# Kernel optimization log

Measured on AMD Instinct MI355X. Metric: run time of the kernel, lower is better.

Reference implementation:

```python
import jax, jax.numpy as jnp
import numpy as np

MEL = 80  # seq2seq_dim


def gru_step(x, h, Wg, bg, Wc, bc):
    """TF GRUCell: gates=[r,u], new_h = u*h + (1-u)*c."""
    gates = jax.nn.sigmoid(jnp.concatenate([x, h], axis=-1) @ Wg + bg)
    r, u = jnp.split(gates, 2, axis=-1)
    c = jnp.tanh(jnp.concatenate([x, r * h], axis=-1) @ Wc + bc)
    return u * h + (1.0 - u) * c


def setup_inputs() -> dict:
    key = jax.random.key(0)
    B, T_enc, D_enc = 128, 1024, 256
    n_styles, style_dim = 10, 256
    reduc, T_dec = 5, 250
    ks = jax.random.split(key, 20)
    rn = lambda k, shape, s=0.05: jax.random.normal(k, shape, jnp.float32) * s
    return {
        "encoder_output": rn(ks[0], (B, T_enc, D_enc), 1.0),
        "inp_mask": jax.random.randint(ks[1], (B,), 1, T_enc + 1, dtype=jnp.int32),
        "inp_att": jax.nn.softmax(rn(ks[2], (B, n_styles), 1.0), axis=-1),
        "style_token": rn(ks[3], (n_styles, style_dim)),
        # decoder prenet 80->256->128
        "pre_W1": rn(ks[4], (MEL, 256)), "pre_b1": jnp.zeros((256,), jnp.float32),
        "pre_W2": rn(ks[5], (256, 128)), "pre_b2": jnp.zeros((128,), jnp.float32),
        # attention GRU cell: input = [context(256), prenet(128)] = 384, hidden 256
        "att_Wg": rn(ks[6], (384 + 256, 512)), "att_bg": jnp.ones((512,), jnp.float32),
        "att_Wc": rn(ks[7], (384 + 256, 256)), "att_bc": jnp.zeros((256,), jnp.float32),
        # Bahdanau attention (depth 256)
        "attn_Wk": rn(ks[8], (256, 256)), "attn_bk": jnp.zeros((256,), jnp.float32),
        "attn_Wq": rn(ks[9], (256, 256)), "attn_bq": jnp.zeros((256,), jnp.float32),
        "attn_v": rn(ks[10], (256,)),
        # dec_input dense: [att_out(256), weighting_context(256)] -> 256
        "deci_W": rn(ks[11], (512, 256)), "deci_b": jnp.zeros((256,), jnp.float32),
        # two residual GRU decoder layers (hidden 256)
        "dec1_Wg": rn(ks[12], (512, 512)), "dec1_bg": jnp.ones((512,), jnp.float32),
        "dec1_Wc": rn(ks[13], (512, 256)), "dec1_bc": jnp.zeros((256,), jnp.float32),
        "dec2_Wg": rn(ks[14], (512, 512)), "dec2_bg": jnp.ones((512,), jnp.float32),
        "dec2_Wc": rn(ks[15], (512, 256)), "dec2_bc": jnp.zeros((256,), jnp.float32),
        # output projection 256 -> mel*reduc
        "out_W": rn(ks[16], (256, MEL * reduc)), "out_b": jnp.zeros((MEL * reduc,), jnp.float32),
        "decode_time_steps": T_dec,
    }


def reference(encoder_output, inp_mask, inp_att, style_token,
              pre_W1, pre_b1, pre_W2, pre_b2,
              att_Wg, att_bg, att_Wc, att_bc,
              attn_Wk, attn_bk, attn_Wq, attn_bq, attn_v,
              deci_W, deci_b,
              dec1_Wg, dec1_bg, dec1_Wc, dec1_bc,
              dec2_Wg, dec2_bg, dec2_Wc, dec2_bc,
              out_W, out_b, decode_time_steps):
    B, T_enc, D = encoder_output.shape
    reduc = out_W.shape[1] // MEL
    # precompute attention keys and mask (done once in TF AttentionModule)
    keys = encoder_output @ attn_Wk + attn_bk                       # [B, T_enc, 256]
    mask = jnp.arange(T_enc)[None, :] < inp_mask[:, None]           # [B, T_enc]
    sentence_style = inp_att @ style_token                          # [B, 256]
    abs_style = jnp.abs(sentence_style)

    carry0 = (
        jnp.zeros((B, 256), jnp.float32),   # att GRU state
        jnp.zeros((B, 256), jnp.float32),   # dec GRU layer 1 state
        jnp.zeros((B, 256), jnp.float32),   # dec GRU layer 2 state
        jnp.zeros((B, 256), jnp.float32),   # last context
        jnp.zeros((B, MEL), jnp.float32),   # go frame / last output
    )

    def step(carry, _):
        h_att, h1, h2, ctx, last_out = carry
        # decoder prenet (dropout inactive, training=False)
        p = jax.nn.relu(last_out @ pre_W1 + pre_b1)
        p = jax.nn.relu(p @ pre_W2 + pre_b2)
        # attention RNN
        h_att = gru_step(jnp.concatenate([ctx, p], axis=-1), h_att,
                         att_Wg, att_bg, att_Wc, att_bc)
        # Bahdanau attention with query = attention cell state
        q = h_att @ attn_Wq + attn_bq                               # [B, 256]
        e = jnp.einsum('btd,d->bt', jnp.tanh(keys + q[:, None, :]), attn_v)
        e = jnp.where(mask, e, -1e9)
        alpha = jax.nn.softmax(e, axis=-1)                          # [B, T_enc]
        context = jnp.einsum('bt,btd->bd', alpha, encoder_output)   # [B, 256]
        # style-weighted context
        wctx = context + sentence_style
        weight_per = jnp.mean(abs_style / (jnp.abs(context) + abs_style))
        # decoder RNN: dense then 2 residual GRU layers
        dec_in = jnp.concatenate([h_att, wctx], axis=-1) @ deci_W + deci_b
        h1 = gru_step(dec_in, h1, dec1_Wg, dec1_bg, dec1_Wc, dec1_bc)
        o1 = h1 + dec_in
        h2 = gru_step(o1, h2, dec2_Wg, dec2_bg, dec2_Wc, dec2_bc)
        o2 = h2 + o1
        dense_out = o2 @ out_W + out_b                              # [B, mel*reduc]
        new_out = dense_out[:, -MEL:]
        return (h_att, h1, h2, context, new_out), (dense_out, alpha, weight_per)

    _, (dense_outs, alphas, weight_pers) = jax.lax.scan(
        step, carry0, None, length=decode_time_steps)
    # [T_dec, B, mel*reduc] -> [B, T_dec*reduc, mel]
    seq2seq_output = jnp.transpose(dense_outs, (1, 0, 2)).reshape(
        B, decode_time_steps * reduc, MEL)
    return seq2seq_output, alphas, weight_pers
```

## Files before the change

kernel.cpp:

```cpp
#include <hip/hip_runtime.h>
#include <cstdint>
#include <cstddef>


#define TDEC   250
#define BATCH  128

#define ALPHA_OFF  ((size_t)12800000)
#define WP_OFF     ((size_t)45568000)

#define WS_WACC_B   ((size_t)0)
#define WS_WGT_B    ((size_t)4096)
#define WGT_ELEMS   1658880
#define WS_KEYS_B   (WS_WGT_B + (size_t)WGT_ELEMS * 2)
#define WS_ENC_B    (WS_KEYS_B + (size_t)33554432 * 2)

#define OFF_PRE_W1   0
#define OFF_PRE_W2   20480
#define OFF_ATT_WG   53248
#define OFF_ATT_WC   380928
#define OFF_ATT_WCH  479232
#define OFF_ATTN_WQ  544768
#define OFF_DECI_W   610304
#define OFF_DEC1_WG  741376
#define OFF_DEC1_WC  1003520
#define OFF_DEC1_WCH 1069056
#define OFF_DEC2_WG  1134592
#define OFF_DEC2_WC  1396736
#define OFF_DEC2_WCH 1462272
#define OFF_OUT_WP   1527808

__device__ inline float bf2f(unsigned short u){
    return __uint_as_float(((unsigned int)u) << 16);
}
__device__ inline unsigned short f2bf(float f){
    unsigned int u = __float_as_uint(f);
    u = (u + 0x7fffu + ((u >> 16) & 1u)) >> 16;
    return (unsigned short)u;
}
__device__ inline float ftanh(float x){
    float e = __expf(2.f * x);
    return 1.f - 2.f * __builtin_amdgcn_rcpf(e + 1.f);
}
__device__ inline float fsig(float x){
    return __builtin_amdgcn_rcpf(1.f + __expf(-x));
}

template<int K, int N, int PARTS>
__device__ inline void gemv_part(const unsigned short* __restrict__ W,
                                 const float* __restrict__ x,
                                 float* __restrict__ scratch, int tid)
{
    constexpr int CH   = N / 8;
    constexpr int LG   = (CH == 16) ? 4 : (CH == 32) ? 5 : 6;
    constexpr int KCNT = K / PARTS;
    static_assert(KCNT * PARTS == K, "K must divide");
    static_assert(CH * PARTS <= 1024, "too many threads");
    const int chunk = tid & (CH - 1);
    const int part  = tid >> LG;
    if (PARTS == (1024 >> LG) || part < PARTS){
        const uint4* Wp = (const uint4*)W + (size_t)(part * KCNT) * (N / 8) + chunk;
        const float* xp = x + part * KCNT;
        float a0=0.f,a1=0.f,a2=0.f,a3=0.f,a4=0.f,a5=0.f,a6=0.f,a7=0.f;
        #pragma unroll 8
        for (int k = 0; k < KCNT; k++){
            uint4 w = Wp[(size_t)k * (N / 8)];
            float xv = xp[k];
            a0 = fmaf(__uint_as_float(w.x << 16),         xv, a0);
            a1 = fmaf(__uint_as_float(w.x & 0xffff0000u), xv, a1);
            a2 = fmaf(__uint_as_float(w.y << 16),         xv, a2);
            a3 = fmaf(__uint_as_float(w.y & 0xffff0000u), xv, a3);
            a4 = fmaf(__uint_as_float(w.z << 16),         xv, a4);
            a5 = fmaf(__uint_as_float(w.z & 0xffff0000u), xv, a5);
            a6 = fmaf(__uint_as_float(w.w << 16),         xv, a6);
            a7 = fmaf(__uint_as_float(w.w & 0xffff0000u), xv, a7);
        }
        float4* s4 = (float4*)(scratch + part * N + chunk * 8);
        s4[0] = float4{a0, a1, a2, a3};
        s4[1] = float4{a4, a5, a6, a7};
    }
}

template<int N, int PARTS>
__device__ inline float red_parts(const float* __restrict__ scratch, int n){
    float s = 0.f;
    #pragma unroll
    for (int p = 0; p < PARTS; p++) s += scratch[p * N + n];
    return s;
}

__global__ void k_cvt_flat(const float* __restrict__ src, unsigned short* __restrict__ dst, int n){
    int i = blockIdx.x * 256 + threadIdx.x;
    if (i < n) dst[i] = f2bf(src[i]);
}
__global__ void k_cvt_pad(const float* __restrict__ src, unsigned short* __restrict__ dst){
    int i = blockIdx.x * 256 + threadIdx.x;
    int k = i >> 9, n = i & 511;
    dst[i] = (n < 400) ? f2bf(src[k * 400 + n]) : (unsigned short)0;
}

__global__ __launch_bounds__(256) void k_keys(const float* __restrict__ enc,
                                              const float* __restrict__ Wk,
                                              const float* __restrict__ bk,
                                              unsigned short* __restrict__ keysT)
{
    __shared__ __align__(16) float Wt[64 * 256];
    __shared__ float At[64 * 64];
    __shared__ unsigned short tileT[256 * 68];
    const int tid = threadIdx.x;
    const size_t row0 = (size_t)blockIdx.x * 64;
    const int dq = tid & 63;
    const int rg = tid >> 6;

    float4 acc[16];
    #pragma unroll
    for (int i = 0; i < 16; i++) acc[i] = float4{0.f, 0.f, 0.f, 0.f};

    for (int k0 = 0; k0 < 256; k0 += 64){
        __syncthreads();
        #pragma unroll
        for (int i = 0; i < 64; i++)
            Wt[i * 256 + tid] = Wk[(size_t)(k0 + i) * 256 + tid];
        #pragma unroll
        for (int i = 0; i < 16; i++){
            int idx = tid + i * 256;
            int r = idx >> 6, kk = idx & 63;
            At[idx] = enc[(row0 + r) * 256 + k0 + kk];
        }
        __syncthreads();
        for (int kk = 0; kk < 64; kk++){
            float4 w = ((const float4*)Wt)[kk * 64 + dq];
            #pragma unroll
            for (int rr = 0; rr < 16; rr++){
                float a = At[(rg * 16 + rr) * 64 + kk];
                acc[rr].x += a * w.x; acc[rr].y += a * w.y;
                acc[rr].z += a * w.z; acc[rr].w += a * w.w;
            }
        }
    }
    float4 bb = ((const float4*)bk)[dq];
    __syncthreads();
    #pragma unroll
    for (int rr = 0; rr < 16; rr++){
        int t_loc = rg * 16 + rr;
        #pragma unroll
        for (int c = 0; c < 4; c++){
            float val = (&acc[rr].x)[c] + (&bb.x)[c];
            int d = dq * 4 + c;
            tileT[d * 68 + t_loc] = f2bf(val);
        }
    }
    __syncthreads();
    const int b_ = (int)(row0 >> 10);
    const int t0 = (int)(row0 & 1023);
    #pragma unroll
    for (int i = 0; i < 16; i++){
        int flat = tid + i * 256;
        int d = flat >> 4, tq = flat & 15;
        ushort4 v = *(const ushort4*)&tileT[d * 68 + tq * 4];
        *(ushort4*)&keysT[(((size_t)(b_ * 256 + d)) << 10) + t0 + tq * 4] = v;
    }
}

struct KParams {
    const int *imask; const float *inp_att; const float *style_tok;
    const float *pre_b1, *pre_b2, *att_bg, *att_bc, *attn_bq, *attn_v;
    const float *deci_b, *dec1_bg, *dec1_bc, *dec2_bg, *dec2_bc, *out_b;
    const unsigned short *wgt;
    const unsigned short *keysT;
    const unsigned short *encb;
    float *wacc; float *out;
};

__global__ __launch_bounds__(1024, 1) void k_main(KParams p)
{
    __shared__ __align__(16) float scr [8192];
    __shared__ __align__(16) float scr2[8192];
    __shared__ float xa[640];
    __shared__ float xg[512];
    __shared__ float xr[256];
    __shared__ float xd[512];
    __shared__ float g_l[512], cx_l[256];
    __shared__ float h_att[256], h1[256], h2[256];
    __shared__ float p1_l[256], dci[256], o1_l[256], o2_l[256];
    __shared__ float stylel[256], astylel[256], v_l[256], q_l[256];
    __shared__ float e_l[1024];
    __shared__ float last_o[80];
    __shared__ float red[16];

    const int tid = threadIdx.x;
    const int b   = blockIdx.x;
    const int mlen = p.imask[b];
    const unsigned short* W = p.wgt;

    if (tid < 256){
        h_att[tid] = 0.f; h1[tid] = 0.f; h2[tid] = 0.f;
        float s = 0.f;
        #pragma unroll
        for (int k = 0; k < 10; k++) s += p.inp_att[b * 10 + k] * p.style_tok[k * 256 + tid];
        stylel[tid] = s; astylel[tid] = fabsf(s);
        v_l[tid] = p.attn_v[tid];
        xa[tid] = 0.f;
        xa[384 + tid] = 0.f;
    }
    if (tid < 80) last_o[tid] = 0.f;
    __syncthreads();

    for (int s = 0; s < TDEC; s++){
        gemv_part<80, 256, 16>(W + OFF_PRE_W1, last_o, scr, tid);
        __syncthreads();
        if (tid < 256)
            p1_l[tid] = fmaxf(p.pre_b1[tid] + red_parts<256,16>(scr, tid), 0.f);
        __syncthreads();

        gemv_part<256, 128, 64>(W + OFF_PRE_W2, p1_l, scr, tid);
        __syncthreads();
        if (tid < 128)
            xa[256 + tid] = fmaxf(p.pre_b2[tid] + red_parts<128,64>(scr, tid), 0.f);
        __syncthreads();

        gemv_part<640, 512, 16>(W + OFF_ATT_WG, xa, scr,  tid);
        gemv_part<384, 256, 32>(W + OFF_ATT_WC, xa, scr2, tid);
        __syncthreads();
        if (tid < 512){
            float g = fsig(p.att_bg[tid] + red_parts<512,16>(scr, tid));
            g_l[tid] = g;
            if (tid < 256) xr[tid] = g * h_att[tid];
        } else if (tid < 768){
            int n = tid - 512;
            cx_l[n] = p.att_bc[n] + red_parts<256,32>(scr2, n);
        }
        __syncthreads();

        gemv_part<256, 256, 32>(W + OFF_ATT_WCH, xr, scr, tid);
        __syncthreads();
        if (tid < 256){
            float c = ftanh(cx_l[tid] + red_parts<256,32>(scr, tid));
            float u = g_l[256 + tid];
            float h = u * h_att[tid] + (1.f - u) * c;
            h_att[tid] = h;
            xa[384 + tid] = h;
            xd[tid] = h;
        }
        __syncthreads();

        gemv_part<256, 256, 32>(W + OFF_ATTN_WQ, h_att, scr, tid);
        __syncthreads();
        if (tid < 256) q_l[tid] = p.attn_bq[tid] + red_parts<256,32>(scr, tid);
        __syncthreads();

        {
            const int tc   = tid & 127;
            const int part = tid >> 7;
            float acc0=0.f,acc1=0.f,acc2=0.f,acc3=0.f,acc4=0.f,acc5=0.f,acc6=0.f,acc7=0.f;
            if (tc * 8 < mlen){
                const unsigned short* kp = p.keysT + (((size_t)b) << 18)
                                         + ((size_t)(part * 32) << 10) + tc * 8;
                #pragma unroll 16
                for (int dd = 0; dd < 32; dd++){
                    uint4 kv = *(const uint4*)(kp + ((size_t)dd << 10));
                    int d = part * 32 + dd;
                    float qd = q_l[d], vd = v_l[d];
                    acc0 = fmaf(ftanh(__uint_as_float(kv.x << 16)         + qd), vd, acc0);
                    acc1 = fmaf(ftanh(__uint_as_float(kv.x & 0xffff0000u) + qd), vd, acc1);
                    acc2 = fmaf(ftanh(__uint_as_float(kv.y << 16)         + qd), vd, acc2);
                    acc3 = fmaf(ftanh(__uint_as_float(kv.y & 0xffff0000u) + qd), vd, acc3);
                    acc4 = fmaf(ftanh(__uint_as_float(kv.z << 16)         + qd), vd, acc4);
                    acc5 = fmaf(ftanh(__uint_as_float(kv.z & 0xffff0000u) + qd), vd, acc5);
                    acc6 = fmaf(ftanh(__uint_as_float(kv.w << 16)         + qd), vd, acc6);
                    acc7 = fmaf(ftanh(__uint_as_float(kv.w & 0xffff0000u) + qd), vd, acc7);
                }
            }
            float4* s4 = (float4*)(scr + part * 1024 + tc * 8);
            s4[0] = float4{acc0, acc1, acc2, acc3};
            s4[1] = float4{acc4, acc5, acc6, acc7};
        }
        __syncthreads();
        float av = 0.f;
        if (tid < mlen){
            float s8 = 0.f;
            #pragma unroll
            for (int pp = 0; pp < 8; pp++) s8 += scr[pp * 1024 + tid];
            av = __expf(s8);
        }
        {
            float ws = av;
            #pragma unroll
            for (int off = 32; off; off >>= 1) ws += __shfl_xor(ws, off, 64);
            if ((tid & 63) == 0) red[tid >> 6] = ws;
        }
        __syncthreads();
        {
            float tot = 0.f;
            #pragma unroll
            for (int i = 0; i < 16; i++) tot += red[i];
            float alpha = av * __builtin_amdgcn_rcpf(tot);
            e_l[tid] = alpha;
            __builtin_nontemporal_store(alpha,
                &p.out[ALPHA_OFF + (size_t)s * 131072 + ((size_t)b << 10) + tid]);
        }
        __syncthreads();

        {
            const int dc = tid & 31;
            const int tp = tid >> 5;
            float acc0=0.f,acc1=0.f,acc2=0.f,acc3=0.f,acc4=0.f,acc5=0.f,acc6=0.f,acc7=0.f;
            const unsigned short* er = p.encb + (((size_t)b) << 18) + dc * 8;
            #pragma unroll 8
            for (int t = tp; t < mlen; t += 32){
                uint4 ev4 = *(const uint4*)(er + ((size_t)t << 8));
                float al = e_l[t];
                acc0 = fmaf(al, __uint_as_float(ev4.x << 16),         acc0);
                acc1 = fmaf(al, __uint_as_float(ev4.x & 0xffff0000u), acc1);
                acc2 = fmaf(al, __uint_as_float(ev4.y << 16),         acc2);
                acc3 = fmaf(al, __uint_as_float(ev4.y & 0xffff0000u), acc3);
                acc4 = fmaf(al, __uint_as_float(ev4.z << 16),         acc4);
                acc5 = fmaf(al, __uint_as_float(ev4.z & 0xffff0000u), acc5);
                acc6 = fmaf(al, __uint_as_float(ev4.w << 16),         acc6);
                acc7 = fmaf(al, __uint_as_float(ev4.w & 0xffff0000u), acc7);
            }
            float4* s4 = (float4*)(scr + tp * 256 + dc * 8);
            s4[0] = float4{acc0, acc1, acc2, acc3};
            s4[1] = float4{acc4, acc5, acc6, acc7};
        }
        __syncthreads();
        if (tid < 256){
            float cs = red_parts<256,32>(scr, tid);
            xa[tid] = cs;
            xd[256 + tid] = cs + stylel[tid];
            float wpv = astylel[tid] * __builtin_amdgcn_rcpf(fabsf(cs) + astylel[tid]);
            #pragma unroll
            for (int off = 32; off; off >>= 1) wpv += __shfl_xor(wpv, off, 64);
            if ((tid & 63) == 0) atomicAdd(&p.wacc[s], wpv);
        }
        __syncthreads();

        gemv_part<512, 256, 32>(W + OFF_DECI_W, xd, scr, tid);
        __syncthreads();
        if (tid < 256){
            float d = p.deci_b[tid] + red_parts<256,32>(scr, tid);
            dci[tid] = d;
            xg[tid] = d; xg[256 + tid] = h1[tid];
        }
        __syncthreads();

        gemv_part<512, 512, 16>(W + OFF_DEC1_WG, xg, scr,  tid);
        gemv_part<256, 256, 32>(W + OFF_DEC1_WC, xg, scr2, tid);
        __syncthreads();
        if (tid < 512){
            float g = fsig(p.dec1_bg[tid] + red_parts<512,16>(scr, tid));
            g_l[tid] = g;
            if (tid < 256) xr[tid] = g * h1[tid];
        } else if (tid < 768){
            int n = tid - 512;
            cx_l[n] = p.dec1_bc[n] + red_parts<256,32>(scr2, n);
        }
        __syncthreads();

        gemv_part<256, 256, 32>(W + OFF_DEC1_WCH, xr, scr, tid);
        __syncthreads();
        if (tid < 256){
            float c = ftanh(cx_l[tid] + red_parts<256,32>(scr, tid));
            float u = g_l[256 + tid];
            float hn = u * h1[tid] + (1.f - u) * c;
            h1[tid] = hn;
            float o1 = hn + dci[tid];
            o1_l[tid] = o1;
            xg[tid] = o1; xg[256 + tid] = h2[tid];
        }
        __syncthreads();

        gemv_part<512, 512, 16>(W + OFF_DEC2_WG, xg, scr,  tid);
        gemv_part<256, 256, 32>(W + OFF_DEC2_WC, xg, scr2, tid);
        __syncthreads();
        if (tid < 512){
            float g = fsig(p.dec2_bg[tid] + red_parts<512,16>(scr, tid));
            g_l[tid] = g;
            if (tid < 256) xr[tid] = g * h2[tid];
        } else if (tid < 768){
            int n = tid - 512;
            cx_l[n] = p.dec2_bc[n] + red_parts<256,32>(scr2, n);
        }
        __syncthreads();

        gemv_part<256, 256, 32>(W + OFF_DEC2_WCH, xr, scr, tid);
        __syncthreads();
        if (tid < 256){
            float c = ftanh(cx_l[tid] + red_parts<256,32>(scr, tid));
            float u = g_l[256 + tid];
            float hn = u * h2[tid] + (1.f - u) * c;
            h2[tid] = hn;
            o2_l[tid] = hn + o1_l[tid];
        }
        __syncthreads();

        gemv_part<256, 512, 16>(W + OFF_OUT_WP, o2_l, scr, tid);
        __syncthreads();
        if (tid < 400){
            float val = p.out_b[tid] + red_parts<512,16>(scr, tid);
            __builtin_nontemporal_store(val,
                &p.out[(size_t)b * 100000 + (size_t)s * 400 + tid]);
            if (tid >= 320) last_o[tid - 320] = val;
        }
        __syncthreads();
    }
}

__global__ void k_final(const float* __restrict__ wacc, float* __restrict__ out)
{
    int i = threadIdx.x;
    if (i < TDEC) out[WP_OFF + i] = wacc[i] * (1.0f / 32768.0f);
}

extern "C" void kernel_launch(void* const* d_in, const int* in_sizes, int n_in,
                              void* d_out, int out_size, void* d_ws, size_t ws_size,
                              hipStream_t stream)
{
    const float* enc        = (const float*)d_in[0];
    const int*   imask      = (const int*)  d_in[1];
    const float* inp_att    = (const float*)d_in[2];
    const float* style_tok  = (const float*)d_in[3];
    const float* pre_W1     = (const float*)d_in[4];
    const float* pre_b1     = (const float*)d_in[5];
    const float* pre_W2     = (const float*)d_in[6];
    const float* pre_b2     = (const float*)d_in[7];
    const float* att_Wg     = (const float*)d_in[8];
    const float* att_bg     = (const float*)d_in[9];
    const float* att_Wc     = (const float*)d_in[10];
    const float* att_bc     = (const float*)d_in[11];
    const float* attn_Wk    = (const float*)d_in[12];
    const float* attn_bk    = (const float*)d_in[13];
    const float* attn_Wq    = (const float*)d_in[14];
    const float* attn_bq    = (const float*)d_in[15];
    const float* attn_v     = (const float*)d_in[16];
    const float* deci_W     = (const float*)d_in[17];
    const float* deci_b     = (const float*)d_in[18];
    const float* dec1_Wg    = (const float*)d_in[19];
    const float* dec1_bg    = (const float*)d_in[20];
    const float* dec1_Wc    = (const float*)d_in[21];
    const float* dec1_bc    = (const float*)d_in[22];
    const float* dec2_Wg    = (const float*)d_in[23];
    const float* dec2_bg    = (const float*)d_in[24];
    const float* dec2_Wc    = (const float*)d_in[25];
    const float* dec2_bc    = (const float*)d_in[26];
    const float* out_W      = (const float*)d_in[27];
    const float* out_b      = (const float*)d_in[28];

    float*          wacc  = (float*)((char*)d_ws + WS_WACC_B);
    unsigned short* wgt   = (unsigned short*)((char*)d_ws + WS_WGT_B);
    unsigned short* keysT = (unsigned short*)((char*)d_ws + WS_KEYS_B);
    unsigned short* encb  = (unsigned short*)((char*)d_ws + WS_ENC_B);
    float* out = (float*)d_out;

    hipMemsetAsync(d_ws, 0, 1024, stream);

    auto cvt = [&](const float* src, size_t off, int n){
        k_cvt_flat<<<(n + 255) / 256, 256, 0, stream>>>(src, wgt + off, n);
    };
    cvt(pre_W1,  OFF_PRE_W1,   80 * 256);
    cvt(pre_W2,  OFF_PRE_W2,  256 * 128);
    cvt(att_Wg,  OFF_ATT_WG,  640 * 512);
    cvt(att_Wc,  OFF_ATT_WC,  640 * 256);
    cvt(attn_Wq, OFF_ATTN_WQ, 256 * 256);
    cvt(deci_W,  OFF_DECI_W,  512 * 256);
    cvt(dec1_Wg, OFF_DEC1_WG, 512 * 512);
    cvt(dec1_Wc, OFF_DEC1_WC, 512 * 256);
    cvt(dec2_Wg, OFF_DEC2_WG, 512 * 512);
    cvt(dec2_Wc, OFF_DEC2_WC, 512 * 256);
    k_cvt_pad<<<(256 * 512) / 256, 256, 0, stream>>>(out_W, wgt + OFF_OUT_WP);

    k_cvt_flat<<<(33554432 + 255) / 256, 256, 0, stream>>>(enc, encb, 33554432);

    k_keys<<<2048, 256, 0, stream>>>(enc, attn_Wk, attn_bk, keysT);

    KParams kp{imask, inp_att, style_tok,
               pre_b1, pre_b2, att_bg, att_bc, attn_bq, attn_v,
               deci_b, dec1_bg, dec1_bc, dec2_bg, dec2_bc, out_b,
               wgt, keysT, encb, wacc, out};
    k_main<<<BATCH, 1024, 0, stream>>>(kp);

    k_final<<<1, 256, 0, stream>>>(wacc, out);
}
```

Measured before the change: 23.70 ms.

## Split each batch row across two workgroups with global-memory pair handshakes

The persistent decoder kernel now runs two 512-thread workgroups per batch element instead of one 1024-thread workgroup. Each half computes its share of the GEMV output columns (or K-rows, for the dec2 and output layers) and its half of the attention time range. The halves exchange partial results through a global comm buffer and spin on per-pair flags. The dec2 gate weights are row-permuted so the K-split fits the concatenated input. This spreads the sequential recurrence over twice as many CUs to cut per-step latency, but adds about nine cross-workgroup syncs per step through L2, and it relies on both halves being co-resident so the spin-wait cannot deadlock.

```diff
diff --git a/kernel.cpp b/kernel.cpp
--- a/kernel.cpp
+++ b/kernel.cpp
@@ -10,10 +10,24 @@
 #define WP_OFF     ((size_t)45568000)
 
 #define WS_WACC_B   ((size_t)0)
-#define WS_WGT_B    ((size_t)4096)
+#define WS_FLAG_B   ((size_t)1024)
+#define WS_COMM_B   ((size_t)4096)
+#define COMM_STRIDE 4096
+#define WS_WGT_B    (WS_COMM_B + (size_t)256 * COMM_STRIDE * 4)
 #define WGT_ELEMS   1658880
 #define WS_KEYS_B   (WS_WGT_B + (size_t)WGT_ELEMS * 2)
 #define WS_ENC_B    (WS_KEYS_B + (size_t)33554432 * 2)
+
+#define CO_E0 0
+#define CO_E1 128
+#define CO_E2 192
+#define CO_E3 576
+#define CO_E4 960
+#define CO_E5 1024
+#define CO_E6 1280
+#define CO_E7 1408
+#define CO_E8 1792
+#define CO_E9 2688
 
 #define OFF_PRE_W1   0
 #define OFF_PRE_W2   20480
@@ -30,9 +44,6 @@
 #define OFF_DEC2_WCH 1462272
 #define OFF_OUT_WP   1527808
 
-__device__ inline float bf2f(unsigned short u){
-    return __uint_as_float(((unsigned int)u) << 16);
-}
 __device__ inline unsigned short f2bf(float f){
     unsigned int u = __float_as_uint(f);
     u = (u + 0x7fffu + ((u >> 16) & 1u)) >> 16;
@@ -46,25 +57,42 @@
     return __builtin_amdgcn_rcpf(1.f + __expf(-x));
 }
 
-template<int K, int N, int PARTS>
-__device__ inline void gemv_part(const unsigned short* __restrict__ W,
-                                 const float* __restrict__ x,
-                                 float* __restrict__ scratch, int tid)
+__device__ inline void cput(float* cm, int i, float v){
+    __hip_atomic_store(cm + i, v, __ATOMIC_RELAXED, __HIP_MEMORY_SCOPE_AGENT);
+}
+__device__ inline float cget(const float* cm, int i){
+    return __hip_atomic_load(cm + i, __ATOMIC_RELAXED, __HIP_MEMORY_SCOPE_AGENT);
+}
+__device__ inline void pair_wait(int* flags, int fm, int fo, int T, int tid){
+    __syncthreads();
+    if (tid == 0){
+        __hip_atomic_store(&flags[fm], T, __ATOMIC_RELAXED, __HIP_MEMORY_SCOPE_AGENT);
+        asm volatile("" ::: "memory");
+        while (__hip_atomic_load(&flags[fo], __ATOMIC_RELAXED, __HIP_MEMORY_SCOPE_AGENT) < T)
+            __builtin_amdgcn_s_sleep(1);
+    }
+    __syncthreads();
+}
+
+template<int K, int NFULL, int NW, int PARTS>
+__device__ inline void gemv_h(const unsigned short* __restrict__ W,
+                              const float* __restrict__ x,
+                              float* __restrict__ scratch, int tid)
 {
-    constexpr int CH   = N / 8;
-    constexpr int LG   = (CH == 16) ? 4 : (CH == 32) ? 5 : 6;
+    constexpr int CH = NW / 8;
+    constexpr int LG = (CH == 8) ? 3 : (CH == 16) ? 4 : (CH == 32) ? 5 : 6;
     constexpr int KCNT = K / PARTS;
     static_assert(KCNT * PARTS == K, "K must divide");
-    static_assert(CH * PARTS <= 1024, "too many threads");
+    static_assert(CH * PARTS <= 512, "too many threads");
     const int chunk = tid & (CH - 1);
     const int part  = tid >> LG;
-    if (PARTS == (1024 >> LG) || part < PARTS){
-        const uint4* Wp = (const uint4*)W + (size_t)(part * KCNT) * (N / 8) + chunk;
+    if (PARTS == (512 >> LG) || part < PARTS){
+        const uint4* Wp = (const uint4*)W + (size_t)(part * KCNT) * (NFULL / 8) + chunk;
         const float* xp = x + part * KCNT;
         float a0=0.f,a1=0.f,a2=0.f,a3=0.f,a4=0.f,a5=0.f,a6=0.f,a7=0.f;
         #pragma unroll 8
         for (int k = 0; k < KCNT; k++){
-            uint4 w = Wp[(size_t)k * (N / 8)];
+            uint4 w = Wp[(size_t)k * (NFULL / 8)];
             float xv = xp[k];
             a0 = fmaf(__uint_as_float(w.x << 16),         xv, a0);
             a1 = fmaf(__uint_as_float(w.x & 0xffff0000u), xv, a1);
@@ -75,17 +103,17 @@
             a6 = fmaf(__uint_as_float(w.w << 16),         xv, a6);
             a7 = fmaf(__uint_as_float(w.w & 0xffff0000u), xv, a7);
         }
-        float4* s4 = (float4*)(scratch + part * N + chunk * 8);
+        float4* s4 = (float4*)(scratch + part * NW + chunk * 8);
         s4[0] = float4{a0, a1, a2, a3};
         s4[1] = float4{a4, a5, a6, a7};
     }
 }
 
-template<int N, int PARTS>
+template<int NW, int PARTS>
 __device__ inline float red_parts(const float* __restrict__ scratch, int n){
     float s = 0.f;
     #pragma unroll
-    for (int p = 0; p < PARTS; p++) s += scratch[p * N + n];
+    for (int p = 0; p < PARTS; p++) s += scratch[p * NW + n];
     return s;
 }
 
@@ -97,6 +125,14 @@
     int i = blockIdx.x * 256 + threadIdx.x;
     int k = i >> 9, n = i & 511;
     dst[i] = (n < 400) ? f2bf(src[k * 400 + n]) : (unsigned short)0;
+}
+__global__ void k_cvt_wg2(const float* __restrict__ src, unsigned short* __restrict__ dst){
+    int i = blockIdx.x * 256 + threadIdx.x;
+    int r = i >> 9, n = i & 511;
+    int c = r >> 7;
+    int nc = (c == 1) ? 2 : (c == 2) ? 1 : c;
+    int nr = nc * 128 + (r & 127);
+    dst[nr * 512 + n] = f2bf(src[i]);
 }
 
 __global__ __launch_bounds__(256) void k_keys(const float* __restrict__ enc,
@@ -169,239 +205,299 @@
     const unsigned short *wgt;
     const unsigned short *keysT;
     const unsigned short *encb;
-    float *wacc; float *out;
+    float *wacc; float *comm; int *flags; float *out;
 };
 
-__global__ __launch_bounds__(1024, 1) void k_main(KParams p)
+__global__ __launch_bounds__(512, 4) void k_main(KParams p)
 {
-    __shared__ __align__(16) float scr [8192];
-    __shared__ __align__(16) float scr2[8192];
+    __shared__ __align__(16) float scr [4096];
+    __shared__ __align__(16) float scr2[4096];
     __shared__ float xa[640];
-    __shared__ float xg[512];
-    __shared__ float xr[256];
-    __shared__ float xd[512];
+    __shared__ float xbuf[512];
     __shared__ float g_l[512], cx_l[256];
-    __shared__ float h_att[256], h1[256], h2[256];
-    __shared__ float p1_l[256], dci[256], o1_l[256], o2_l[256];
+    __shared__ float h1[256], h2[256], dci[256], o1_l[256], o2loc[128];
+    __shared__ float p1_l[256];
     __shared__ float stylel[256], astylel[256], v_l[256], q_l[256];
-    __shared__ float e_l[1024];
+    __shared__ float e_l[512];
     __shared__ float last_o[80];
     __shared__ float red[16];
 
     const int tid = threadIdx.x;
-    const int b   = blockIdx.x;
+    const int b   = blockIdx.x >> 1;
+    const int h   = blockIdx.x & 1;
     const int mlen = p.imask[b];
     const unsigned short* W = p.wgt;
 
+    float* cm = p.comm + (size_t)(2 * b + h) * COMM_STRIDE;
+    const float* co = p.comm + (size_t)(2 * b + (1 - h)) * COMM_STRIDE;
+    const int fm = 2 * b + h, fo = 2 * b + (1 - h);
+    int seq = 0;
+
     if (tid < 256){
-        h_att[tid] = 0.f; h1[tid] = 0.f; h2[tid] = 0.f;
+        xa[384 + tid] = 0.f;
+        xa[tid] = 0.f;
+        h1[tid] = 0.f; h2[tid] = 0.f;
         float s = 0.f;
         #pragma unroll
         for (int k = 0; k < 10; k++) s += p.inp_att[b * 10 + k] * p.style_tok[k * 256 + tid];
         stylel[tid] = s; astylel[tid] = fabsf(s);
         v_l[tid] = p.attn_v[tid];
-        xa[tid] = 0.f;
-        xa[384 + tid] = 0.f;
     }
     if (tid < 80) last_o[tid] = 0.f;
     __syncthreads();
 
     for (int s = 0; s < TDEC; s++){
-        gemv_part<80, 256, 16>(W + OFF_PRE_W1, last_o, scr, tid);
-        __syncthreads();
+        gemv_h<80, 256, 128, 16>(W + OFF_PRE_W1 + h * 128, last_o, scr, tid);
+        __syncthreads();
+        if (tid < 128){
+            float v = fmaxf(p.pre_b1[h * 128 + tid] + red_parts<128,16>(scr, tid), 0.f);
+            p1_l[h * 128 + tid] = v;
+            cput(cm, CO_E0 + tid, v);
+        }
+        pair_wait(p.flags, fm, fo, ++seq, tid);
+        if (tid < 128) p1_l[(1 - h) * 128 + tid] = cget(co, CO_E0 + tid);
+        __syncthreads();
+
+        gemv_h<256, 128, 64, 64>(W + OFF_PRE_W2 + h * 64, p1_l, scr, tid);
+        __syncthreads();
+        if (tid < 64){
+            float v = fmaxf(p.pre_b2[h * 64 + tid] + red_parts<64,64>(scr, tid), 0.f);
+            xa[256 + h * 64 + tid] = v;
+            cput(cm, CO_E1 + tid, v);
+        }
+        pair_wait(p.flags, fm, fo, ++seq, tid);
+        if (tid < 64) xa[256 + (1 - h) * 64 + tid] = cget(co, CO_E1 + tid);
+        __syncthreads();
+
+        gemv_h<640, 512, 256, 16>(W + OFF_ATT_WG + h * 256, xa, scr,  tid);
+        gemv_h<384, 256, 128, 32>(W + OFF_ATT_WC + h * 128, xa, scr2, tid);
+        __syncthreads();
+        if (tid < 256){
+            float g = fsig(p.att_bg[h * 256 + tid] + red_parts<256,16>(scr, tid));
+            g_l[h * 256 + tid] = g;
+            cput(cm, CO_E2 + tid, g);
+        }
+        if (tid < 128){
+            float cx = p.att_bc[h * 128 + tid] + red_parts<128,32>(scr2, tid);
+            cx_l[h * 128 + tid] = cx;
+            cput(cm, CO_E2 + 256 + tid, cx);
+        }
+        pair_wait(p.flags, fm, fo, ++seq, tid);
+        if (tid < 256) g_l[(1 - h) * 256 + tid] = cget(co, CO_E2 + tid);
+        if (tid < 128) cx_l[(1 - h) * 128 + tid] = cget(co, CO_E2 + 256 + tid);
+        __syncthreads();
+
+        if (tid < 256) xbuf[tid] = g_l[tid] * xa[384 + tid];
+        __syncthreads();
+        gemv_h<256, 256, 128, 32>(W + OFF_ATT_WCH + h * 128, xbuf, scr, tid);
+        __syncthreads();
+        if (tid < 128){
+            int n = h * 128 + tid;
+            float c = ftanh(cx_l[n] + red_parts<128,32>(scr, tid));
+            float u = g_l[256 + n];
+            xa[384 + n] = u * xa[384 + n] + (1.f - u) * c;
+        }
+        __syncthreads();
+
+        gemv_h<128, 256, 256, 16>(W + OFF_ATTN_WQ + (size_t)(h * 128) * 256,
+                                  &xa[384 + h * 128], scr2, tid);
+        __syncthreads();
+        if (tid < 128) cput(cm, CO_E3 + tid, xa[384 + h * 128 + tid]);
+        if (tid < 256) cput(cm, CO_E3 + 128 + tid, red_parts<256,16>(scr2, tid));
+        pair_wait(p.flags, fm, fo, ++seq, tid);
+        if (tid < 128) xa[384 + (1 - h) * 128 + tid] = cget(co, CO_E3 + tid);
         if (tid < 256)
-            p1_l[tid] = fmaxf(p.pre_b1[tid] + red_parts<256,16>(scr, tid), 0.f);
-        __syncthreads();
-
-        gemv_part<256, 128, 64>(W + OFF_PRE_W2, p1_l, scr, tid);
-        __syncthreads();
-        if (tid < 128)
-            xa[256 + tid] = fmaxf(p.pre_b2[tid] + red_parts<128,64>(scr, tid), 0.f);
-        __syncthreads();
-
-        gemv_part<640, 512, 16>(W + OFF_ATT_WG, xa, scr,  tid);
-        gemv_part<384, 256, 32>(W + OFF_ATT_WC, xa, scr2, tid);
-        __syncthreads();
-        if (tid < 512){
-            float g = fsig(p.att_bg[tid] + red_parts<512,16>(scr, tid));
-            g_l[tid] = g;
-            if (tid < 256) xr[tid] = g * h_att[tid];
-        } else if (tid < 768){
-            int n = tid - 512;
-            cx_l[n] = p.att_bc[n] + red_parts<256,32>(scr2, n);
-        }
-        __syncthreads();
-
-        gemv_part<256, 256, 32>(W + OFF_ATT_WCH, xr, scr, tid);
-        __syncthreads();
-        if (tid < 256){
-            float c = ftanh(cx_l[tid] + red_parts<256,32>(scr, tid));
-            float u = g_l[256 + tid];
-            float h = u * h_att[tid] + (1.f - u) * c;
-            h_att[tid] = h;
-            xa[384 + tid] = h;
-            xd[tid] = h;
-        }
-        __syncthreads();
-
-        gemv_part<256, 256, 32>(W + OFF_ATTN_WQ, h_att, scr, tid);
-        __syncthreads();
-        if (tid < 256) q_l[tid] = p.attn_bq[tid] + red_parts<256,32>(scr, tid);
+            q_l[tid] = p.attn_bq[tid] + red_parts<256,16>(scr2, tid) + cget(co, CO_E3 + 128 + tid);
         __syncthreads();
 
         {
-            const int tc   = tid & 127;
-            const int part = tid >> 7;
-            float acc0=0.f,acc1=0.f,acc2=0.f,acc3=0.f,acc4=0.f,acc5=0.f,acc6=0.f,acc7=0.f;
-            if (tc * 8 < mlen){
+            const int tc   = tid & 63;
+            const int part = tid >> 6;
+            float a0=0.f,a1=0.f,a2=0.f,a3=0.f,a4=0.f,a5=0.f,a6=0.f,a7=0.f;
+            if (h * 512 + tc * 8 < mlen){
                 const unsigned short* kp = p.keysT + (((size_t)b) << 18)
-                                         + ((size_t)(part * 32) << 10) + tc * 8;
+                                         + ((size_t)(part * 32) << 10) + h * 512 + tc * 8;
                 #pragma unroll 16
                 for (int dd = 0; dd < 32; dd++){
                     uint4 kv = *(const uint4*)(kp + ((size_t)dd << 10));
                     int d = part * 32 + dd;
                     float qd = q_l[d], vd = v_l[d];
-                    acc0 = fmaf(ftanh(__uint_as_float(kv.x << 16)         + qd), vd, acc0);
-                    acc1 = fmaf(ftanh(__uint_as_float(kv.x & 0xffff0000u) + qd), vd, acc1);
-                    acc2 = fmaf(ftanh(__uint_as_float(kv.y << 16)         + qd), vd, acc2);
-                    acc3 = fmaf(ftanh(__uint_as_float(kv.y & 0xffff0000u) + qd), vd, acc3);
-                    acc4 = fmaf(ftanh(__uint_as_float(kv.z << 16)         + qd), vd, acc4);
-                    acc5 = fmaf(ftanh(__uint_as_float(kv.z & 0xffff0000u) + qd), vd, acc5);
-                    acc6 = fmaf(ftanh(__uint_as_float(kv.w << 16)         + qd), vd, acc6);
-                    acc7 = fmaf(ftanh(__uint_as_float(kv.w & 0xffff0000u) + qd), vd, acc7);
+                    a0 = fmaf(ftanh(__uint_as_float(kv.x << 16)         + qd), vd, a0);
+                    a1 = fmaf(ftanh(__uint_as_float(kv.x & 0xffff0000u) + qd), vd, a1);
+                    a2 = fmaf(ftanh(__uint_as_float(kv.y << 16)         + qd), vd, a2);
+                    a3 = fmaf(ftanh(__uint_as_float(kv.y & 0xffff0000u) + qd), vd, a3);
+                    a4 = fmaf(ftanh(__uint_as_float(kv.z << 16)         + qd), vd, a4);
+                    a5 = fmaf(ftanh(__uint_as_float(kv.z & 0xffff0000u) + qd), vd, a5);
+                    a6 = fmaf(ftanh(__uint_as_float(kv.w << 16)         + qd), vd, a6);
+                    a7 = fmaf(ftanh(__uint_as_float(kv.w & 0xffff0000u) + qd), vd, a7);
                 }
             }
-            float4* s4 = (float4*)(scr + part * 1024 + tc * 8);
-            s4[0] = float4{acc0, acc1, acc2, acc3};
-            s4[1] = float4{acc4, acc5, acc6, acc7};
-        }
-        __syncthreads();
-        float av = 0.f;
-        if (tid < mlen){
-            float s8 = 0.f;
+            float4* s4 = (float4*)(scr + part * 512 + tc * 8);
+            s4[0] = float4{a0, a1, a2, a3};
+            s4[1] = float4{a4, a5, a6, a7};
+        }
+        __syncthreads();
+        float av;
+        {
+            float e = 0.f;
             #pragma unroll
-            for (int pp = 0; pp < 8; pp++) s8 += scr[pp * 1024 + tid];
-            av = __expf(s8);
-        }
-        {
+            for (int pp = 0; pp < 8; pp++) e += scr[pp * 512 + tid];
+            av = (h * 512 + tid < mlen) ? __expf(e) : 0.f;
             float ws = av;
             #pragma unroll
             for (int off = 32; off; off >>= 1) ws += __shfl_xor(ws, off, 64);
             if ((tid & 63) == 0) red[tid >> 6] = ws;
         }
         __syncthreads();
+        if (tid == 0){
+            float dl = 0.f;
+            #pragma unroll
+            for (int i = 0; i < 8; i++) dl += red[i];
+            red[8] = dl;
+            cput(cm, CO_E4, dl);
+        }
+        pair_wait(p.flags, fm, fo, ++seq, tid);
         {
-            float tot = 0.f;
-            #pragma unroll
-            for (int i = 0; i < 16; i++) tot += red[i];
-            float alpha = av * __builtin_amdgcn_rcpf(tot);
+            float total = red[8] + cget(co, CO_E4);
+            float alpha = av * __builtin_amdgcn_rcpf(total);
             e_l[tid] = alpha;
             __builtin_nontemporal_store(alpha,
-                &p.out[ALPHA_OFF + (size_t)s * 131072 + ((size_t)b << 10) + tid]);
+                &p.out[ALPHA_OFF + (size_t)s * 131072 + ((size_t)b << 10) + h * 512 + tid]);
         }
         __syncthreads();
 
         {
             const int dc = tid & 31;
             const int tp = tid >> 5;
-            float acc0=0.f,acc1=0.f,acc2=0.f,acc3=0.f,acc4=0.f,acc5=0.f,acc6=0.f,acc7=0.f;
-            const unsigned short* er = p.encb + (((size_t)b) << 18) + dc * 8;
+            float a0=0.f,a1=0.f,a2=0.f,a3=0.f,a4=0.f,a5=0.f,a6=0.f,a7=0.f;
+            int mloc = mlen - h * 512;
+            if (mloc > 512) mloc = 512;
+            const unsigned short* er = p.encb + (((size_t)b) << 18)
+                                     + ((size_t)(h * 512) << 8) + dc * 8;
             #pragma unroll 8
-            for (int t = tp; t < mlen; t += 32){
+            for (int t = tp; t < mloc; t += 16){
                 uint4 ev4 = *(const uint4*)(er + ((size_t)t << 8));
                 float al = e_l[t];
-                acc0 = fmaf(al, __uint_as_float(ev4.x << 16),         acc0);
-                acc1 = fmaf(al, __uint_as_float(ev4.x & 0xffff0000u), acc1);
-                acc2 = fmaf(al, __uint_as_float(ev4.y << 16),         acc2);
-                acc3 = fmaf(al, __uint_as_float(ev4.y & 0xffff0000u), acc3);
-                acc4 = fmaf(al, __uint_as_float(ev4.z << 16),         acc4);
-                acc5 = fmaf(al, __uint_as_float(ev4.z & 0xffff0000u), acc5);
-                acc6 = fmaf(al, __uint_as_float(ev4.w << 16),         acc6);
-                acc7 = fmaf(al, __uint_as_float(ev4.w & 0xffff0000u), acc7);
+                a0 = fmaf(al, __uint_as_float(ev4.x << 16),         a0);
+                a1 = fmaf(al, __uint_as_float(ev4.x & 0xffff0000u), a1);
+                a2 = fmaf(al, __uint_as_float(ev4.y << 16),         a2);
+                a3 = fmaf(al, __uint_as_float(ev4.y & 0xffff0000u), a3);
+                a4 = fmaf(al, __uint_as_float(ev4.z << 16),         a4);
+                a5 = fmaf(al, __uint_as_float(ev4.z & 0xffff0000u), a5);
+                a6 = fmaf(al, __uint_as_float(ev4.w << 16),         a6);
+                a7 = fmaf(al, __uint_as_float(ev4.w & 0xffff0000u), a7);
             }
             float4* s4 = (float4*)(scr + tp * 256 + dc * 8);
-            s4[0] = float4{acc0, acc1, acc2, acc3};
-            s4[1] = float4{acc4, acc5, acc6, acc7};
-        }
-        __syncthreads();
+            s4[0] = float4{a0, a1, a2, a3};
+            s4[1] = float4{a4, a5, a6, a7};
+        }
+        __syncthreads();
+        if (tid < 256) cput(cm, CO_E5 + tid, red_parts<256,16>(scr, tid));
+        pair_wait(p.flags, fm, fo, ++seq, tid);
         if (tid < 256){
-            float cs = red_parts<256,32>(scr, tid);
+            float cs = red_parts<256,16>(scr, tid) + cget(co, CO_E5 + tid);
             xa[tid] = cs;
-            xd[256 + tid] = cs + stylel[tid];
-            float wpv = astylel[tid] * __builtin_amdgcn_rcpf(fabsf(cs) + astylel[tid]);
-            #pragma unroll
-            for (int off = 32; off; off >>= 1) wpv += __shfl_xor(wpv, off, 64);
-            if ((tid & 63) == 0) atomicAdd(&p.wacc[s], wpv);
-        }
-        __syncthreads();
-
-        gemv_part<512, 256, 32>(W + OFF_DECI_W, xd, scr, tid);
+            if (h == 0){
+                float wpv = astylel[tid] * __builtin_amdgcn_rcpf(fabsf(cs) + astylel[tid]);
+                #pragma unroll
+                for (int off = 32; off; off >>= 1) wpv += __shfl_xor(wpv, off, 64);
+                if ((tid & 63) == 0) atomicAdd(&p.wacc[s], wpv);
+            }
+        }
+        __syncthreads();
+
+        xbuf[tid] = (tid < 256) ? xa[384 + tid] : xa[tid - 256] + stylel[tid - 256];
+        __syncthreads();
+        gemv_h<512, 256, 128, 32>(W + OFF_DECI_W + h * 128, xbuf, scr, tid);
+        __syncthreads();
+        if (tid < 128){
+            float d = p.deci_b[h * 128 + tid] + red_parts<128,32>(scr, tid);
+            dci[h * 128 + tid] = d;
+            cput(cm, CO_E6 + tid, d);
+        }
+        pair_wait(p.flags, fm, fo, ++seq, tid);
+        if (tid < 128) dci[(1 - h) * 128 + tid] = cget(co, CO_E6 + tid);
+        __syncthreads();
+
+        xbuf[tid] = (tid < 256) ? dci[tid] : h1[tid - 256];
+        __syncthreads();
+        gemv_h<512, 512, 256, 16>(W + OFF_DEC1_WG + h * 256, xbuf, scr,  tid);
+        gemv_h<256, 256, 128, 32>(W + OFF_DEC1_WC + h * 128, xbuf, scr2, tid);
         __syncthreads();
         if (tid < 256){
-            float d = p.deci_b[tid] + red_parts<256,32>(scr, tid);
-            dci[tid] = d;
-            xg[tid] = d; xg[256 + tid] = h1[tid];
-        }
-        __syncthreads();
-
-        gemv_part<512, 512, 16>(W + OFF_DEC1_WG, xg, scr,  tid);
-        gemv_part<256, 256, 32>(W + OFF_DEC1_WC, xg, scr2, tid);
-        __syncthreads();
-        if (tid < 512){
-            float g = fsig(p.dec1_bg[tid] + red_parts<512,16>(scr, tid));
-            g_l[tid] = g;
-            if (tid < 256) xr[tid] = g * h1[tid];
-        } else if (tid < 768){
-            int n = tid - 512;
-            cx_l[n] = p.dec1_bc[n] + red_parts<256,32>(scr2, n);
-        }
-        __syncthreads();
-
-        gemv_part<256, 256, 32>(W + OFF_DEC1_WCH, xr, scr, tid);
-        __syncthreads();
-        if (tid < 256){
-            float c = ftanh(cx_l[tid] + red_parts<256,32>(scr, tid));
-            float u = g_l[256 + tid];
-            float hn = u * h1[tid] + (1.f - u) * c;
-            h1[tid] = hn;
-            float o1 = hn + dci[tid];
-            o1_l[tid] = o1;
-            xg[tid] = o1; xg[256 + tid] = h2[tid];
-        }
-        __syncthreads();
-
-        gemv_part<512, 512, 16>(W + OFF_DEC2_WG, xg, scr,  tid);
-        gemv_part<256, 256, 32>(W + OFF_DEC2_WC, xg, scr2, tid);
-        __syncthreads();
-        if (tid < 512){
-            float g = fsig(p.dec2_bg[tid] + red_parts<512,16>(scr, tid));
-            g_l[tid] = g;
-            if (tid < 256) xr[tid] = g * h2[tid];
-        } else if (tid < 768){
-            int n = tid - 512;
-            cx_l[n] = p.dec2_bc[n] + red_parts<256,32>(scr2, n);
-        }
-        __syncthreads();
-
-        gemv_part<256, 256, 32>(W + OFF_DEC2_WCH, xr, scr, tid);
-        __syncthreads();
-        if (tid < 256){
-            float c = ftanh(cx_l[tid] + red_parts<256,32>(scr, tid));
-            float u = g_l[256 + tid];
-            float hn = u * h2[tid] + (1.f - u) * c;
-            h2[tid] = hn;
-            o2_l[tid] = hn + o1_l[tid];
-        }
-        __syncthreads();
-
-        gemv_part<256, 512, 16>(W + OFF_OUT_WP, o2_l, scr, tid);
-        __syncthreads();
-        if (tid < 400){
-            float val = p.out_b[tid] + red_parts<512,16>(scr, tid);
-            __builtin_nontemporal_store(val,
-                &p.out[(size_t)b * 100000 + (size_t)s * 400 + tid]);
-            if (tid >= 320) last_o[tid - 320] = val;
-        }
+            float g = fsig(p.dec1_bg[h * 256 + tid] + red_parts<256,16>(scr, tid));
+            g_l[h * 256 + tid] = g;
+            cput(cm, CO_E7 + tid, g);
+        }
+        if (tid < 128){
+            float cx = p.dec1_bc[h * 128 + tid] + red_parts<128,32>(scr2, tid);
+            cx_l[h * 128 + tid] = cx;
+            cput(cm, CO_E7 + 256 + tid, cx);
+        }
+        pair_wait(p.flags, fm, fo, ++seq, tid);
+        if (tid < 256) g_l[(1 - h) * 256 + tid] = cget(co, CO_E7 + tid);
+        if (tid < 128) cx_l[(1 - h) * 128 + tid] = cget(co, CO_E7 + 256 + tid);
+        __syncthreads();
+
+        if (tid < 256) xbuf[tid] = g_l[tid] * h1[tid];
+        __syncthreads();
+        gemv_h<256, 256, 128, 32>(W + OFF_DEC1_WCH + h * 128, xbuf, scr, tid);
+        __syncthreads();
+        if (tid < 128){
+            int n = h * 128 + tid;
+            float c = ftanh(cx_l[n] + red_parts<128,32>(scr, tid));
+            float u = g_l[256 + n];
+            float hn = u * h1[n] + (1.f - u) * c;
+            h1[n] = hn;
+            o1_l[n] = hn + dci[n];
+        }
+        __syncthreads();
+
+        if (tid < 256)
+            xbuf[tid] = (tid < 128) ? o1_l[h * 128 + tid] : h2[h * 128 + (tid - 128)];
+        __syncthreads();
+        gemv_h<256, 512, 512, 8>(W + OFF_DEC2_WG + (size_t)(h * 256) * 512, xbuf, scr, tid);
+        gemv_h<128, 256, 256, 16>(W + OFF_DEC2_WC + (size_t)(h * 128) * 256, xbuf, scr2, tid);
+        __syncthreads();
+        if (tid < 128) cput(cm, CO_E8 + tid, h1[h * 128 + tid]);
+        cput(cm, CO_E8 + 128 + tid, red_parts<512,8>(scr, tid));
+        if (tid < 256) cput(cm, CO_E8 + 640 + tid, red_parts<256,16>(scr2, tid));
+        pair_wait(p.flags, fm, fo, ++seq, tid);
+        g_l[tid] = fsig(p.dec2_bg[tid] + red_parts<512,8>(scr, tid) + cget(co, CO_E8 + 128 + tid));
+        if (tid < 256)
+            cx_l[tid] = p.dec2_bc[tid] + red_parts<256,16>(scr2, tid) + cget(co, CO_E8 + 640 + tid);
+        if (tid < 128) h1[(1 - h) * 128 + tid] = cget(co, CO_E8 + tid);
+        __syncthreads();
+
+        if (tid < 256) xbuf[tid] = g_l[tid] * h2[tid];
+        __syncthreads();
+        gemv_h<256, 256, 128, 32>(W + OFF_DEC2_WCH + h * 128, xbuf, scr, tid);
+        __syncthreads();
+        if (tid < 128){
+            int n = h * 128 + tid;
+            float c = ftanh(cx_l[n] + red_parts<128,32>(scr, tid));
+            float u = g_l[256 + n];
+            float hn = u * h2[n] + (1.f - u) * c;
+            h2[n] = hn;
+            o2loc[tid] = hn + o1_l[n];
+        }
+        __syncthreads();
+
+        gemv_h<128, 512, 512, 8>(W + OFF_OUT_WP + (size_t)(h * 128) * 512, o2loc, scr2, tid);
+        __syncthreads();
+        if (tid < 128) cput(cm, CO_E9 + tid, h2[h * 128 + tid]);
+        cput(cm, CO_E9 + 128 + tid, red_parts<512,8>(scr2, tid));
+        pair_wait(p.flags, fm, fo, ++seq, tid);
+        {
+            float bias = (tid < 400) ? p.out_b[tid] : 0.f;
+            float dv = bias + red_parts<512,8>(scr2, tid) + cget(co, CO_E9 + 128 + tid);
+            if (tid >= 320 && tid < 400) last_o[tid - 320] = dv;
+            bool mine = h ? (tid >= 256 && tid < 400) : (tid < 256);
+            if (mine)
+                __builtin_nontemporal_store(dv,
+                    &p.out[(size_t)b * 100000 + (size_t)s * 400 + tid]);
+        }
+        if (tid < 128) h2[(1 - h) * 128 + tid] = cget(co, CO_E9 + tid);
         __syncthreads();
     }
 }
@@ -447,12 +543,14 @@
     const float* out_b      = (const float*)d_in[28];
 
     float*          wacc  = (float*)((char*)d_ws + WS_WACC_B);
+    int*            flags = (int*)  ((char*)d_ws + WS_FLAG_B);
+    float*          comm  = (float*)((char*)d_ws + WS_COMM_B);
     unsigned short* wgt   = (unsigned short*)((char*)d_ws + WS_WGT_B);
     unsigned short* keysT = (unsigned short*)((char*)d_ws + WS_KEYS_B);
     unsigned short* encb  = (unsigned short*)((char*)d_ws + WS_ENC_B);
     float* out = (float*)d_out;
 
-    hipMemsetAsync(d_ws, 0, 1024, stream);
+    hipMemsetAsync(d_ws, 0, 2048, stream);
 
     auto cvt = [&](const float* src, size_t off, int n){
         k_cvt_flat<<<(n + 255) / 256, 256, 0, stream>>>(src, wgt + off, n);
@@ -465,19 +563,18 @@
     cvt(deci_W,  OFF_DECI_W,  512 * 256);
     cvt(dec1_Wg, OFF_DEC1_WG, 512 * 512);
     cvt(dec1_Wc, OFF_DEC1_WC, 512 * 256);
-    cvt(dec2_Wg, OFF_DEC2_WG, 512 * 512);
+    k_cvt_wg2<<<(512 * 512) / 256, 256, 0, stream>>>(dec2_Wg, wgt + OFF_DEC2_WG);
     cvt(dec2_Wc, OFF_DEC2_WC, 512 * 256);
     k_cvt_pad<<<(256 * 512) / 256, 256, 0, stream>>>(out_W, wgt + OFF_OUT_WP);
 
     k_cvt_flat<<<(33554432 + 255) / 256, 256, 0, stream>>>(enc, encb, 33554432);
-
     k_keys<<<2048, 256, 0, stream>>>(enc, attn_Wk, attn_bk, keysT);
 
     KParams kp{imask, inp_att, style_tok,
                pre_b1, pre_b2, att_bg, att_bc, attn_bq, attn_v,
                deci_b, dec1_bg, dec1_bc, dec2_bg, dec2_bc, out_b,
-               wgt, keysT, encb, wacc, out};
-    k_main<<<BATCH, 1024, 0, stream>>>(kp);
+               wgt, keysT, encb, wacc, comm, flags, out};
+    k_main<<<2 * BATCH, 512, 0, stream>>>(kp);
 
     k_final<<<1, 256, 0, stream>>>(wacc, out);
 }
```

Result: slower. 27.08 ms (+14.3%).
